# Kernel tuning notes

Hardware: AMD Instinct MI355X
Metric: run time of the kernel (lower is better)

Reference implementation:

```python
import jax, jax.numpy as jnp
import numpy as np

B, T, DM, H, DH = 4, 2048, 1024, 16, 64
DI = H * DH
CLIP = 1.0
LN_EPS = 1e-5


def setup_inputs() -> dict:
    key = jax.random.key(0)
    ks = jax.random.split(key, 9)

    def xav(k, shape):  # xavier_uniform, fan_in=shape[1], fan_out=shape[0]
        lim = float(np.sqrt(6.0 / (shape[0] + shape[1])))
        return jax.random.uniform(k, shape, jnp.float32, -lim, lim)

    def kai(k, shape):  # default nn.Linear weight init
        lim = float(1.0 / np.sqrt(shape[1]))
        return jax.random.uniform(k, shape, jnp.float32, -lim, lim)

    return {
        "x": jax.random.normal(ks[0], (B, T, DM), jnp.float32),
        "Wq": xav(ks[1], (DI, DM)),
        "Wk": xav(ks[2], (DI, DM)),
        "Wv": xav(ks[3], (DI, DM)),
        "Wa": kai(ks[4], (DI, DM)), "ba": jnp.full((DI,), 3.0, jnp.float32),
        "Wb": kai(ks[5], (H, DM)), "bb": jnp.zeros((H,), jnp.float32),
        "Wg": kai(ks[6], (H, DM)), "bg": jnp.zeros((H,), jnp.float32),
        "WaR": kai(ks[7], (DI, DM)), "baR": jnp.full((DI,), 3.0, jnp.float32),
        "Wo": xav(ks[8], (DM, DI)),
        "ln_w": jnp.ones((DM,), jnp.float32),
        "ln_b": jnp.zeros((DM,), jnp.float32),
    }


def reference(x, Wq, Wk, Wv, Wa, ba, Wb, bb, Wg, bg, WaR, baR, Wo, ln_w, ln_b):
    Bs, Ts, _ = x.shape
    residual = x
    # LayerNorm
    mu = jnp.mean(x, -1, keepdims=True)
    var = jnp.mean((x - mu) ** 2, -1, keepdims=True)
    xn = (x - mu) / jnp.sqrt(var + LN_EPS) * ln_w + ln_b

    q = (xn @ Wq.T).reshape(Bs, Ts, H, DH)
    k = (xn @ Wk.T).reshape(Bs, Ts, H, DH)
    v = (xn @ Wv.T).reshape(Bs, Ts, H, DH)
    alpha = jax.nn.sigmoid(xn @ Wa.T + ba).reshape(Bs, Ts, H, DH)
    aR = jax.nn.sigmoid(xn @ WaR.T + baR).reshape(Bs, Ts, H, DH)
    beta = jax.nn.sigmoid(xn @ Wb.T + bb)   # (B,T,H)
    gamma = jax.nn.sigmoid(xn @ Wg.T + bg)  # (B,T,H)

    tm = lambda a: jnp.moveaxis(a, 1, 0)  # time-major for scan
    xs = (tm(q), tm(k), tm(v), tm(alpha), tm(aR), tm(beta), tm(gamma))
    S0 = jnp.zeros((Bs, H, DH, DH), x.dtype)

    def step(carry, inp):
        S, R = carry
        q_t, k_t, v_t, a_t, aR_t, b_t, g_t = inp  # (B,H,d) / (B,H)
        kn = k_t / jnp.maximum(jnp.linalg.norm(k_t, axis=-1, keepdims=True), 1e-12)
        # residual target from previous state: r = clip(v - S^T k)
        pred = jnp.einsum('bhji,bhj->bhi', S, kn)
        r = jnp.clip(v_t - pred, -CLIP, CLIP)
        # primary state: S = diag(alpha) S; S += beta k (v - k^T S)
        S = a_t[..., None] * S
        kp = jnp.einsum('bhd,bhde->bhe', kn, S)
        S = S + b_t[..., None, None] * kn[..., None] * (v_t - kp)[..., None, :]
        o = jnp.einsum('bhji,bhj->bhi', S, q_t)
        # residual state
        R = aR_t[..., None] * R
        kpR = jnp.einsum('bhd,bhde->bhe', kn, R)
        R = R + g_t[..., None, None] * kn[..., None] * (r - kpR)[..., None, :]
        o = o + jnp.einsum('bhji,bhj->bhi', R, q_t)
        return (S, R), o

    _, os = jax.lax.scan(step, (S0, S0), xs)  # os: (T,B,H,d)
    out = jnp.moveaxis(os, 0, 1).reshape(Bs, Ts, DI) @ Wo.T
    return out + residual  # dropout is identity at inference
```

## Files before the change

### kernel.cpp

```cpp
#include <hip/hip_runtime.h>
#include <hip/hip_fp16.h>

#define B_SZ 4
#define T_SEQ 2048
#define NH 16
#define HD 64
#define DMODEL 1024
#define MTOT (B_SZ * T_SEQ)

typedef __bf16 bf16x8 __attribute__((ext_vector_type(8)));
typedef float f32x4 __attribute__((ext_vector_type(4)));
typedef float f32x2 __attribute__((ext_vector_type(2)));
typedef _Float16 f16x4 __attribute__((ext_vector_type(4)));

__device__ __forceinline__ unsigned short f2bf(float f) {
    union { float f; unsigned int i; } c; c.f = f;
    unsigned int u = c.i;
    u += 0x7fffu + ((u >> 16) & 1u);
    return (unsigned short)(u >> 16);
}
__device__ __forceinline__ float sigm(float x) { return 1.f / (1.f + __expf(-x)); }

__device__ __forceinline__ void dma16(const void* g, void* l) {
    __builtin_amdgcn_global_load_lds(
        (const __attribute__((address_space(1))) void*)g,
        (__attribute__((address_space(3))) void*)l, 16, 0, 0);
}

template <int CTRL>
__device__ __forceinline__ float dppadd(float x) {
    int v = __builtin_amdgcn_update_dpp(0, __builtin_bit_cast(int, x), CTRL, 0xf, 0xf, false);
    return x + __builtin_bit_cast(float, v);
}
__device__ __forceinline__ float rowsum16(float x) {
    x = dppadd<0x128>(x);
    x = dppadd<0x124>(x);
    x = dppadd<0x122>(x);
    x = dppadd<0x121>(x);
    return x;
}

__global__ __launch_bounds__(256, 1) void k_ln(const float* __restrict__ x,
                                               const float* __restrict__ lnw,
                                               const float* __restrict__ lnb,
                                               unsigned short* __restrict__ xn) {
    const int m = blockIdx.x;
    const int t = threadIdx.x;
    float4 xv = ((const float4*)(x + (size_t)m * DMODEL))[t];
    float s = xv.x + xv.y + xv.z + xv.w;
    float s2 = xv.x * xv.x + xv.y * xv.y + xv.z * xv.z + xv.w * xv.w;
#pragma unroll
    for (int off = 32; off >= 1; off >>= 1) {
        s += __shfl_xor(s, off);
        s2 += __shfl_xor(s2, off);
    }
    __shared__ float red[8];
    const int wid = t >> 6;
    if ((t & 63) == 0) { red[wid] = s; red[4 + wid] = s2; }
    __syncthreads();
    if (t == 0) {
        float su = red[0] + red[1] + red[2] + red[3];
        float sq = red[4] + red[5] + red[6] + red[7];
        float mu = su * (1.f / DMODEL);
        float var = sq * (1.f / DMODEL) - mu * mu;
        red[0] = mu;
        red[1] = rsqrtf(var + 1e-5f);
    }
    __syncthreads();
    float mu = red[0], rstd = red[1];
    float4 w4 = ((const float4*)lnw)[t];
    float4 b4 = ((const float4*)lnb)[t];
    ushort4 o;
    o.x = f2bf((xv.x - mu) * rstd * w4.x + b4.x);
    o.y = f2bf((xv.y - mu) * rstd * w4.y + b4.y);
    o.z = f2bf((xv.z - mu) * rstd * w4.z + b4.z);
    o.w = f2bf((xv.w - mu) * rstd * w4.w + b4.w);
    ((ushort4*)(xn + (size_t)m * DMODEL))[t] = o;
}

struct WPtrs { const float* p0; const float* p1; const float* p2; const float* p3; const float* p4; };

__global__ __launch_bounds__(256, 1) void k_wconv(WPtrs w, unsigned short* __restrict__ dst) {
    const int plane = blockIdx.y;
    const float* src = plane == 0 ? w.p0 : plane == 1 ? w.p1 : plane == 2 ? w.p2
                                                             : plane == 3 ? w.p3 : w.p4;
    const size_t i = ((size_t)blockIdx.x * 256 + threadIdx.x) * 8;
    float4 f0 = *(const float4*)(src + i);
    float4 f1 = *(const float4*)(src + i + 4);
    uint4 o;
    o.x = (unsigned)f2bf(f0.x) | ((unsigned)f2bf(f0.y) << 16);
    o.y = (unsigned)f2bf(f0.z) | ((unsigned)f2bf(f0.w) << 16);
    o.z = (unsigned)f2bf(f1.x) | ((unsigned)f2bf(f1.y) << 16);
    o.w = (unsigned)f2bf(f1.z) | ((unsigned)f2bf(f1.w) << 16);
    *(uint4*)(dst + (size_t)plane * 1048576 + i) = o;
}

__global__ __launch_bounds__(256, 1) void k_cvt1(const float* __restrict__ src,
                                                 unsigned short* __restrict__ dst) {
    const size_t i = ((size_t)blockIdx.x * 256 + threadIdx.x) * 8;
    float4 f0 = *(const float4*)(src + i);
    float4 f1 = *(const float4*)(src + i + 4);
    uint4 o;
    o.x = (unsigned)f2bf(f0.x) | ((unsigned)f2bf(f0.y) << 16);
    o.y = (unsigned)f2bf(f0.z) | ((unsigned)f2bf(f0.w) << 16);
    o.z = (unsigned)f2bf(f1.x) | ((unsigned)f2bf(f1.y) << 16);
    o.w = (unsigned)f2bf(f1.z) | ((unsigned)f2bf(f1.w) << 16);
    *(uint4*)(dst + i) = o;
}

template <int KDIM>
__device__ __forceinline__ void gemm128(const unsigned short* __restrict__ A,
                                        const unsigned short* __restrict__ Bw,
                                        int m0, int n0, f32x4 acc[4][4]) {
    __shared__ __align__(16) unsigned short sA[128 * 32];
    __shared__ __align__(16) unsigned short sB[128 * 32];

    const int t = threadIdx.x;
    const int lane = t & 63;
    const int wv = t >> 6;
    const int wm = wv >> 1, wn = wv & 1;
    const int ml = lane & 15, kq = lane >> 4;

#pragma unroll
    for (int i = 0; i < 4; i++)
#pragma unroll
        for (int j = 0; j < 4; j++) {
            f32x4 z; z[0] = 0.f; z[1] = 0.f; z[2] = 0.f; z[3] = 0.f;
            acc[i][j] = z;
        }

    const unsigned short* pA = A + (size_t)m0 * KDIM;
    const unsigned short* pB = Bw + (size_t)n0 * KDIM;
    const unsigned short* gA0 = pA + (size_t)(t >> 2) * KDIM + (t & 3) * 8;
    const unsigned short* gA1 = gA0 + (size_t)64 * KDIM;
    const unsigned short* gB0 = pB + (size_t)(t >> 2) * KDIM + (t & 3) * 8;
    const unsigned short* gB1 = gB0 + (size_t)64 * KDIM;
    unsigned short* lA0 = sA + wv * 512;
    unsigned short* lA1 = lA0 + 2048;
    unsigned short* lB0 = sB + wv * 512;
    unsigned short* lB1 = lB0 + 2048;

    for (int kb = 0; kb < KDIM / 32; kb++) {
        const int ko = kb * 32;
        dma16(gA0 + ko, lA0);
        dma16(gA1 + ko, lA1);
        dma16(gB0 + ko, lB0);
        dma16(gB1 + ko, lB1);
        __syncthreads();
        bf16x8 af[4], bfr[4];
#pragma unroll
        for (int mt = 0; mt < 4; mt++)
            af[mt] = *(const bf16x8*)&sA[(wm * 64 + mt * 16 + ml) * 32 + kq * 8];
#pragma unroll
        for (int nt = 0; nt < 4; nt++)
            bfr[nt] = *(const bf16x8*)&sB[(wn * 64 + nt * 16 + ml) * 32 + kq * 8];
#pragma unroll
        for (int mt = 0; mt < 4; mt++)
#pragma unroll
            for (int nt = 0; nt < 4; nt++)
                acc[mt][nt] = __builtin_amdgcn_mfma_f32_16x16x32_bf16(af[mt], bfr[nt], acc[mt][nt], 0, 0, 0);
        __syncthreads();
    }
}

__global__ __launch_bounds__(256, 1) void k_proj(const unsigned short* __restrict__ xn,
                                                 const unsigned short* __restrict__ wbf,
                                                 const float* __restrict__ ba,
                                                 const float* __restrict__ baR,
                                                 __half* __restrict__ qo, __half* __restrict__ ko,
                                                 __half* __restrict__ vo, __half* __restrict__ ao,
                                                 __half* __restrict__ aRo) {
    const int m0 = blockIdx.x * 128;
    const int yt = blockIdx.y;
    const int widx = yt >> 3;
    const int n0 = (yt & 7) * 128;
    const unsigned short* W = wbf + (size_t)widx * 1048576;
    f32x4 acc[4][4];
    gemm128<1024>(xn, W, m0, n0, acc);

    __half* outp = widx == 0 ? qo : widx == 1 ? ko : widx == 2 ? vo : widx == 3 ? ao : aRo;
    const float* bias = (widx == 3) ? ba : (widx == 4) ? baR : (const float*)0;
    const int lane = threadIdx.x & 63;
    const int wv = threadIdx.x >> 6;
    const int wm = wv >> 1, wn = wv & 1;
    const int ml = lane & 15, kq = lane >> 4;
#pragma unroll
    for (int mt = 0; mt < 4; mt++)
#pragma unroll
        for (int nt = 0; nt < 4; nt++) {
            const int rowg = m0 + wm * 64 + mt * 16 + kq * 4;
            const int colg = n0 + wn * 64 + nt * 16 + ml;
            float bval = bias ? bias[colg] : 0.f;
#pragma unroll
            for (int r = 0; r < 4; r++) {
                float v = acc[mt][nt][r];
                if (widx >= 3) v = sigm(v + bval);
                outp[(size_t)(rowg + r) * DMODEL + colg] = __float2half(v);
            }
        }
}

__global__ __launch_bounds__(256, 1) void k_bg(const unsigned short* __restrict__ xn,
                                               const float* __restrict__ Wb,
                                               const float* __restrict__ bb,
                                               const float* __restrict__ Wg,
                                               const float* __restrict__ bgp,
                                               f32x2* __restrict__ bgpk) {
    const int m = blockIdx.x;
    const int t = threadIdx.x;
    const int h = t >> 4, seg = t & 15;
    const ushort4* xr = (const ushort4*)(xn + (size_t)m * DMODEL + seg * 64);
    const float4* wbr = (const float4*)(Wb + (size_t)h * DMODEL + seg * 64);
    const float4* wgr = (const float4*)(Wg + (size_t)h * DMODEL + seg * 64);
    float db = 0.f, dg = 0.f;
#pragma unroll
    for (int u = 0; u < 16; u++) {
        ushort4 a = xr[u];
        float4 w1 = wbr[u], w2 = wgr[u];
        union { unsigned int i; float f; } c0, c1, c2, c3;
        c0.i = ((unsigned int)a.x) << 16; c1.i = ((unsigned int)a.y) << 16;
        c2.i = ((unsigned int)a.z) << 16; c3.i = ((unsigned int)a.w) << 16;
        db += c0.f * w1.x + c1.f * w1.y + c2.f * w1.z + c3.f * w1.w;
        dg += c0.f * w2.x + c1.f * w2.y + c2.f * w2.z + c3.f * w2.w;
    }
#pragma unroll
    for (int off = 1; off < 16; off <<= 1) {
        db += __shfl_xor(db, off);
        dg += __shfl_xor(dg, off);
    }
    if (seg == 0) {
        f32x2 o;
        o[0] = sigm(db + bb[h]);
        o[1] = sigm(dg + bgp[h]);
        bgpk[(size_t)m * NH + h] = o;
    }
}

__global__ __launch_bounds__(256, 1) void k_prep(__half* __restrict__ kb) {
    const int row = blockIdx.x * 16 + (threadIdx.x >> 4);
    const int tr = threadIdx.x & 15;
    const int bh = row >> 11, t = row & 2047;
    const size_t idx = ((size_t)((bh >> 4) * T_SEQ + t)) * DMODEL + (bh & 15) * 64 + tr * 4;
    f16x4 k4 = *(const f16x4*)((const __half*)kb + idx);
    float k0 = (float)k4[0], k1 = (float)k4[1], k2 = (float)k4[2], k3 = (float)k4[3];
    float ss = k0 * k0 + k1 * k1 + k2 * k2 + k3 * k3;
    ss = rowsum16(ss);
    float inv = 1.f / fmaxf(sqrtf(ss), 1e-12f);
    f16x4 o;
    o[0] = (_Float16)(k0 * inv); o[1] = (_Float16)(k1 * inv);
    o[2] = (_Float16)(k2 * inv); o[3] = (_Float16)(k3 * inv);
    *(f16x4*)(kb + idx) = o;
}

__global__ __launch_bounds__(256, 1) void k_scan(const __half* __restrict__ qb,
                                                 const __half* __restrict__ knb,
                                                 const __half* __restrict__ vb,
                                                 const __half* __restrict__ ab,
                                                 const __half* __restrict__ aRb,
                                                 const f32x2* __restrict__ bgpk,
                                                 unsigned short* __restrict__ ob) {
    const int blk = blockIdx.x;
    const int bh = blk & 63, cg = blk >> 6;
    const int b = bh >> 4, h = bh & 15;
    const int t = threadIdx.x;
    const int col = t >> 4, tr = t & 15;
    const int ii = cg * 16 + col;
    const int j0 = tr * 4;

    const size_t vecbase = ((size_t)b * T_SEQ) * DMODEL + h * 64 + j0;
    const size_t vbase = ((size_t)b * T_SEQ) * DMODEL + h * 64 + ii;
    const size_t bgbase = ((size_t)b * T_SEQ) * NH + h;

    const __half* pk = knb + vecbase;
    const __half* pq = qb + vecbase;
    const __half* pa = ab + vecbase;
    const __half* pr = aRb + vecbase;

    float S0 = 0, S1 = 0, S2 = 0, S3 = 0, R0 = 0, R1 = 0, R2 = 0, R3 = 0;

    f16x4 rk[6], rq[6], ra[6], rr[6];
    __half rv[6];
    f32x2 rbg[6];
    f32x4 fkn[6], fq[6], fa[6], fr[6];
    float fv[6];

#pragma unroll
    for (int p = 0; p < 6; p++) {
        const size_t voff = (size_t)p * DMODEL;
        rk[p] = *(const f16x4*)(pk + voff);
        rq[p] = *(const f16x4*)(pq + voff);
        ra[p] = *(const f16x4*)(pa + voff);
        rr[p] = *(const f16x4*)(pr + voff);
        rv[p] = vb[vbase + voff];
        rbg[p] = bgpk[bgbase + (size_t)p * NH];
    }
    fkn[0][0] = (float)rk[0][0]; fkn[0][1] = (float)rk[0][1]; fkn[0][2] = (float)rk[0][2]; fkn[0][3] = (float)rk[0][3];
    fq[0][0] = (float)rq[0][0]; fq[0][1] = (float)rq[0][1]; fq[0][2] = (float)rq[0][2]; fq[0][3] = (float)rq[0][3];
    fa[0][0] = (float)ra[0][0]; fa[0][1] = (float)ra[0][1]; fa[0][2] = (float)ra[0][2]; fa[0][3] = (float)ra[0][3];
    fr[0][0] = (float)rr[0][0]; fr[0][1] = (float)rr[0][1]; fr[0][2] = (float)rr[0][2]; fr[0][3] = (float)rr[0][3];
    fv[0] = (float)rv[0];

#define SCAN_BODY(P, PN)                                                              \
    {                                                                                 \
        const int s = st + (P);                                                       \
        const float beta = rbg[P][0], gamma = rbg[P][1];                              \
                     \
        {                                                                             \
            const size_t voff = (size_t)((s + 6) & (T_SEQ - 1)) * DMODEL;             \
            rk[P] = *(const f16x4*)(pk + voff);                                       \
            rq[P] = *(const f16x4*)(pq + voff);                                       \
            ra[P] = *(const f16x4*)(pa + voff);                                       \
            rr[P] = *(const f16x4*)(pr + voff);                                       \
            rv[P] = vb[vbase + voff];                                                 \
        }                                                                             \
                                    \
        fkn[PN][0] = (float)rk[PN][0]; fkn[PN][1] = (float)rk[PN][1];                 \
        fkn[PN][2] = (float)rk[PN][2]; fkn[PN][3] = (float)rk[PN][3];                 \
        fq[PN][0] = (float)rq[PN][0]; fq[PN][1] = (float)rq[PN][1];                   \
        fq[PN][2] = (float)rq[PN][2]; fq[PN][3] = (float)rq[PN][3];                   \
        fa[PN][0] = (float)ra[PN][0]; fa[PN][1] = (float)ra[PN][1];                   \
        fa[PN][2] = (float)ra[PN][2]; fa[PN][3] = (float)ra[PN][3];                   \
        fr[PN][0] = (float)rr[PN][0]; fr[PN][1] = (float)rr[PN][1];                   \
        fr[PN][2] = (float)rr[PN][2]; fr[PN][3] = (float)rr[PN][3];                   \
        fv[PN] = (float)rv[PN];                                                       \
                                          \
        {                                                                             \
            const float kn0 = fkn[P][0], kn1 = fkn[P][1], kn2 = fkn[P][2], kn3 = fkn[P][3]; \
            const float a0 = fa[P][0], a1 = fa[P][1], a2 = fa[P][2], a3 = fa[P][3];   \
            const float x0 = fr[P][0], x1 = fr[P][1], x2 = fr[P][2], x3 = fr[P][3];   \
            const float vc = fv[P];                                                   \
            float pred = S0 * kn0 + S1 * kn1 + S2 * kn2 + S3 * kn3;                   \
            float Sd0 = a0 * S0, Sd1 = a1 * S1, Sd2 = a2 * S2, Sd3 = a3 * S3;         \
            float Rd0 = x0 * R0, Rd1 = x1 * R1, Rd2 = x2 * R2, Rd3 = x3 * R3;         \
            float kp = Sd0 * kn0 + Sd1 * kn1 + Sd2 * kn2 + Sd3 * kn3;                 \
            float kpR = Rd0 * kn0 + Rd1 * kn1 + Rd2 * kn2 + Rd3 * kn3;                \
            pred = rowsum16(pred);                                                    \
            kp = rowsum16(kp);                                                        \
            kpR = rowsum16(kpR);                                                      \
            const float rres = fminf(fmaxf(vc - pred, -1.f), 1.f);                    \
            const float cS = beta * (vc - kp);                                        \
            const float cR = gamma * (rres - kpR);                                    \
            S0 = fmaf(cS, kn0, Sd0); S1 = fmaf(cS, kn1, Sd1);                         \
            S2 = fmaf(cS, kn2, Sd2); S3 = fmaf(cS, kn3, Sd3);                         \
            R0 = fmaf(cR, kn0, Rd0); R1 = fmaf(cR, kn1, Rd1);                         \
            R2 = fmaf(cR, kn2, Rd2); R3 = fmaf(cR, kn3, Rd3);                         \
            float o = (S0 + R0) * fq[P][0] + (S1 + R1) * fq[P][1] +                   \
                      (S2 + R2) * fq[P][2] + (S3 + R3) * fq[P][3];                    \
            o = rowsum16(o);                                                          \
            if (tr == 0 && s < T_SEQ)                                                 \
                ob[vbase + (size_t)s * DMODEL] = f2bf(o);                             \
        }                                                                             \
             \
        rbg[P] = bgpk[bgbase + (size_t)((s + 6) & (T_SEQ - 1)) * NH];                 \
    }

    for (int st = 0; st < T_SEQ; st += 6) {
        SCAN_BODY(0, 1)
        SCAN_BODY(1, 2)
        SCAN_BODY(2, 3)
        SCAN_BODY(3, 4)
        SCAN_BODY(4, 5)
        SCAN_BODY(5, 0)
    }
#undef SCAN_BODY
}

__global__ __launch_bounds__(256, 1) void k_out(const unsigned short* __restrict__ ob,
                                                const unsigned short* __restrict__ wobf,
                                                const float* __restrict__ x,
                                                float* __restrict__ out) {
    const int m0 = blockIdx.x * 128;
    const int n0 = blockIdx.y * 128;
    f32x4 acc[4][4];
    gemm128<1024>(ob, wobf, m0, n0, acc);
    const int lane = threadIdx.x & 63;
    const int wv = threadIdx.x >> 6;
    const int wm = wv >> 1, wn = wv & 1;
    const int ml = lane & 15, kq = lane >> 4;
#pragma unroll
    for (int mt = 0; mt < 4; mt++)
#pragma unroll
        for (int nt = 0; nt < 4; nt++) {
            const int rowg = m0 + wm * 64 + mt * 16 + kq * 4;
            const int colg = n0 + wn * 64 + nt * 16 + ml;
#pragma unroll
            for (int r = 0; r < 4; r++) {
                size_t idx = (size_t)(rowg + r) * DMODEL + colg;
                out[idx] = acc[mt][nt][r] + x[idx];
            }
        }
}

extern "C" void kernel_launch(void* const* d_in, const int* in_sizes, int n_in,
                              void* d_out, int out_size, void* d_ws, size_t ws_size,
                              hipStream_t stream) {
    const float* x = (const float*)d_in[0];
    const float* Wq = (const float*)d_in[1];
    const float* Wk = (const float*)d_in[2];
    const float* Wv = (const float*)d_in[3];
    const float* Wa = (const float*)d_in[4];
    const float* ba = (const float*)d_in[5];
    const float* Wb = (const float*)d_in[6];
    const float* bb = (const float*)d_in[7];
    const float* Wg = (const float*)d_in[8];
    const float* bg = (const float*)d_in[9];
    const float* WaR = (const float*)d_in[10];
    const float* baR = (const float*)d_in[11];
    const float* Wo = (const float*)d_in[12];
    const float* lnw = (const float*)d_in[13];
    const float* lnb = (const float*)d_in[14];

    const size_t SZ = 16777216ULL;
    size_t need = 6 * SZ + 2 * 1048576ULL;
    if (ws_size < need) return;

    char* ws = (char*)d_ws;
    __half* qb = (__half*)(ws + 0 * SZ);
    __half* kb = (__half*)(ws + 1 * SZ);
    __half* vb = (__half*)(ws + 2 * SZ);
    __half* ab = (__half*)(ws + 3 * SZ);
    __half* aRb = (__half*)(ws + 4 * SZ);
    unsigned short* xn = (unsigned short*)(ws + 5 * SZ);
    f32x2* bgpk = (f32x2*)(ws + 6 * SZ);

    unsigned short* wbf = (unsigned short*)d_out;
    unsigned short* wobf = (unsigned short*)qb;

    WPtrs wp{Wq, Wk, Wv, Wa, WaR};
    k_wconv<<<dim3(512, 5), dim3(256), 0, stream>>>(wp, wbf);
    k_ln<<<dim3(MTOT), dim3(256), 0, stream>>>(x, lnw, lnb, xn);
    k_proj<<<dim3(64, 40), dim3(256), 0, stream>>>(xn, wbf, ba, baR, qb, kb, vb, ab, aRb);
    k_bg<<<dim3(MTOT), dim3(256), 0, stream>>>(xn, Wb, bb, Wg, bg, bgpk);
    k_prep<<<dim3(MTOT * NH / 16), dim3(256), 0, stream>>>(kb);
    k_scan<<<dim3(256), dim3(256), 0, stream>>>(qb, kb, vb, ab, aRb, bgpk, xn);
    k_cvt1<<<dim3(512), dim3(256), 0, stream>>>(Wo, wobf);
    k_out<<<dim3(64, 8), dim3(256), 0, stream>>>(xn, wobf, x, (float*)d_out);
}
```

Before: 944.4 us.

## Run recurrent scan on MFMA with fp16 state in single wavefront blocks

The scan kernel now runs each 16-column state slice in one 64-lane wavefront instead of a 256-thread block. State S and R are held as fp16 vectors (16 rows per lane across 4 quads). The k^T S, k^T R and q^T S dot products use 16x16x32 fp16 MFMA instructions in place of DPP row reductions. This cuts the per-step cross-lane reduction latency on the serial critical path. The trade-off is fp16 storage of the recurrent state, which risks accumulated precision loss over 2048 steps, and MFMA issue latency on each step.

```diff
diff --git a/kernel.cpp b/kernel.cpp
--- a/kernel.cpp
+++ b/kernel.cpp
@@ -12,6 +12,7 @@
 typedef float f32x4 __attribute__((ext_vector_type(4)));
 typedef float f32x2 __attribute__((ext_vector_type(2)));
 typedef _Float16 f16x4 __attribute__((ext_vector_type(4)));
+typedef _Float16 f16x8 __attribute__((ext_vector_type(8)));
 
 __device__ __forceinline__ unsigned short f2bf(float f) {
     union { float f; unsigned int i; } c; c.f = f;
@@ -252,117 +253,86 @@
     *(f16x4*)(kb + idx) = o;
 }
 
-__global__ __launch_bounds__(256, 1) void k_scan(const __half* __restrict__ qb,
-                                                 const __half* __restrict__ knb,
-                                                 const __half* __restrict__ vb,
-                                                 const __half* __restrict__ ab,
-                                                 const __half* __restrict__ aRb,
-                                                 const f32x2* __restrict__ bgpk,
-                                                 unsigned short* __restrict__ ob) {
+__global__ __launch_bounds__(64, 1) void k_scan(const __half* __restrict__ qb,
+                                                const __half* __restrict__ knb,
+                                                const __half* __restrict__ vb,
+                                                const __half* __restrict__ ab,
+                                                const __half* __restrict__ aRb,
+                                                const f32x2* __restrict__ bgpk,
+                                                unsigned short* __restrict__ ob) {
     const int blk = blockIdx.x;
     const int bh = blk & 63, cg = blk >> 6;
     const int b = bh >> 4, h = bh & 15;
-    const int t = threadIdx.x;
-    const int col = t >> 4, tr = t & 15;
+    const int l = threadIdx.x;
+    const int col = l & 15, quad = l >> 4;
     const int ii = cg * 16 + col;
-    const int j0 = tr * 4;
-
-    const size_t vecbase = ((size_t)b * T_SEQ) * DMODEL + h * 64 + j0;
-    const size_t vbase = ((size_t)b * T_SEQ) * DMODEL + h * 64 + ii;
-    const size_t bgbase = ((size_t)b * T_SEQ) * NH + h;
-
-    const __half* pk = knb + vecbase;
-    const __half* pq = qb + vecbase;
-    const __half* pa = ab + vecbase;
-    const __half* pr = aRb + vecbase;
-
-    float S0 = 0, S1 = 0, S2 = 0, S3 = 0, R0 = 0, R1 = 0, R2 = 0, R3 = 0;
-
-    f16x4 rk[6], rq[6], ra[6], rr[6];
-    __half rv[6];
-    f32x2 rbg[6];
-    f32x4 fkn[6], fq[6], fa[6], fr[6];
-    float fv[6];
-
-#pragma unroll
-    for (int p = 0; p < 6; p++) {
-        const size_t voff = (size_t)p * DMODEL;
-        rk[p] = *(const f16x4*)(pk + voff);
-        rq[p] = *(const f16x4*)(pq + voff);
-        ra[p] = *(const f16x4*)(pa + voff);
-        rr[p] = *(const f16x4*)(pr + voff);
-        rv[p] = vb[vbase + voff];
-        rbg[p] = bgpk[bgbase + (size_t)p * NH];
-    }
-    fkn[0][0] = (float)rk[0][0]; fkn[0][1] = (float)rk[0][1]; fkn[0][2] = (float)rk[0][2]; fkn[0][3] = (float)rk[0][3];
-    fq[0][0] = (float)rq[0][0]; fq[0][1] = (float)rq[0][1]; fq[0][2] = (float)rq[0][2]; fq[0][3] = (float)rq[0][3];
-    fa[0][0] = (float)ra[0][0]; fa[0][1] = (float)ra[0][1]; fa[0][2] = (float)ra[0][2]; fa[0][3] = (float)ra[0][3];
-    fr[0][0] = (float)rr[0][0]; fr[0][1] = (float)rr[0][1]; fr[0][2] = (float)rr[0][2]; fr[0][3] = (float)rr[0][3];
-    fv[0] = (float)rv[0];
-
-#define SCAN_BODY(P, PN)                                                              \
-    {                                                                                 \
-        const int s = st + (P);                                                       \
-        const float beta = rbg[P][0], gamma = rbg[P][1];                              \
-                     \
-        {                                                                             \
-            const size_t voff = (size_t)((s + 6) & (T_SEQ - 1)) * DMODEL;             \
-            rk[P] = *(const f16x4*)(pk + voff);                                       \
-            rq[P] = *(const f16x4*)(pq + voff);                                       \
-            ra[P] = *(const f16x4*)(pa + voff);                                       \
-            rr[P] = *(const f16x4*)(pr + voff);                                       \
-            rv[P] = vb[vbase + voff];                                                 \
-        }                                                                             \
-                                    \
-        fkn[PN][0] = (float)rk[PN][0]; fkn[PN][1] = (float)rk[PN][1];                 \
-        fkn[PN][2] = (float)rk[PN][2]; fkn[PN][3] = (float)rk[PN][3];                 \
-        fq[PN][0] = (float)rq[PN][0]; fq[PN][1] = (float)rq[PN][1];                   \
-        fq[PN][2] = (float)rq[PN][2]; fq[PN][3] = (float)rq[PN][3];                   \
-        fa[PN][0] = (float)ra[PN][0]; fa[PN][1] = (float)ra[PN][1];                   \
-        fa[PN][2] = (float)ra[PN][2]; fa[PN][3] = (float)ra[PN][3];                   \
-        fr[PN][0] = (float)rr[PN][0]; fr[PN][1] = (float)rr[PN][1];                   \
-        fr[PN][2] = (float)rr[PN][2]; fr[PN][3] = (float)rr[PN][3];                   \
-        fv[PN] = (float)rv[PN];                                                       \
-                                          \
-        {                                                                             \
-            const float kn0 = fkn[P][0], kn1 = fkn[P][1], kn2 = fkn[P][2], kn3 = fkn[P][3]; \
-            const float a0 = fa[P][0], a1 = fa[P][1], a2 = fa[P][2], a3 = fa[P][3];   \
-            const float x0 = fr[P][0], x1 = fr[P][1], x2 = fr[P][2], x3 = fr[P][3];   \
-            const float vc = fv[P];                                                   \
-            float pred = S0 * kn0 + S1 * kn1 + S2 * kn2 + S3 * kn3;                   \
-            float Sd0 = a0 * S0, Sd1 = a1 * S1, Sd2 = a2 * S2, Sd3 = a3 * S3;         \
-            float Rd0 = x0 * R0, Rd1 = x1 * R1, Rd2 = x2 * R2, Rd3 = x3 * R3;         \
-            float kp = Sd0 * kn0 + Sd1 * kn1 + Sd2 * kn2 + Sd3 * kn3;                 \
-            float kpR = Rd0 * kn0 + Rd1 * kn1 + Rd2 * kn2 + Rd3 * kn3;                \
-            pred = rowsum16(pred);                                                    \
-            kp = rowsum16(kp);                                                        \
-            kpR = rowsum16(kpR);                                                      \
-            const float rres = fminf(fmaxf(vc - pred, -1.f), 1.f);                    \
-            const float cS = beta * (vc - kp);                                        \
-            const float cR = gamma * (rres - kpR);                                    \
-            S0 = fmaf(cS, kn0, Sd0); S1 = fmaf(cS, kn1, Sd1);                         \
-            S2 = fmaf(cS, kn2, Sd2); S3 = fmaf(cS, kn3, Sd3);                         \
-            R0 = fmaf(cR, kn0, Rd0); R1 = fmaf(cR, kn1, Rd1);                         \
-            R2 = fmaf(cR, kn2, Rd2); R3 = fmaf(cR, kn3, Rd3);                         \
-            float o = (S0 + R0) * fq[P][0] + (S1 + R1) * fq[P][1] +                   \
-                      (S2 + R2) * fq[P][2] + (S3 + R3) * fq[P][3];                    \
-            o = rowsum16(o);                                                          \
-            if (tr == 0 && s < T_SEQ)                                                 \
-                ob[vbase + (size_t)s * DMODEL] = f2bf(o);                             \
-        }                                                                             \
-             \
-        rbg[P] = bgpk[bgbase + (size_t)((s + 6) & (T_SEQ - 1)) * NH];                 \
-    }
-
-    for (int st = 0; st < T_SEQ; st += 6) {
-        SCAN_BODY(0, 1)
-        SCAN_BODY(1, 2)
-        SCAN_BODY(2, 3)
-        SCAN_BODY(3, 4)
-        SCAN_BODY(4, 5)
-        SCAN_BODY(5, 0)
-    }
-#undef SCAN_BODY
+
+    const size_t base = (size_t)b * T_SEQ * DMODEL + h * 64;
+    const __half* pk = knb + base + quad * 8;
+    const __half* pq = qb + base + quad * 8;
+    const __half* pa = ab + base + quad * 8;
+    const __half* pr = aRb + base + quad * 8;
+    const __half* pv = vb + base + ii;
+    unsigned short* po = ob + base + ii;
+    const size_t bgbase = (size_t)b * T_SEQ * NH + h;
+
+    f16x8 SL = (f16x8)(_Float16)0, SH = (f16x8)(_Float16)0;
+    f16x8 RL = (f16x8)(_Float16)0, RH = (f16x8)(_Float16)0;
+
+    struct In {
+        f16x8 knL, knH, aL, aH, xL, xH, qL, qH;
+        float vc;
+        f32x2 bg;
+    };
+
+    auto load = [&](int s) {
+        In r;
+        const size_t vo = (size_t)s * DMODEL;
+        r.knL = *(const f16x8*)(pk + vo); r.knH = *(const f16x8*)(pk + vo + 32);
+        r.aL = *(const f16x8*)(pa + vo);  r.aH = *(const f16x8*)(pa + vo + 32);
+        r.xL = *(const f16x8*)(pr + vo);  r.xH = *(const f16x8*)(pr + vo + 32);
+        r.qL = *(const f16x8*)(pq + vo);  r.qH = *(const f16x8*)(pq + vo + 32);
+        r.vc = (float)pv[vo];
+        r.bg = bgpk[bgbase + (size_t)s * NH];
+        return r;
+    };
+
+    auto step = [&](const In& c, int s) {
+        f32x4 z; z[0] = 0.f; z[1] = 0.f; z[2] = 0.f; z[3] = 0.f;
+        f32x4 pA1 = __builtin_amdgcn_mfma_f32_16x16x32_f16(c.knL, SL, z, 0, 0, 0);
+        f32x4 pA2 = __builtin_amdgcn_mfma_f32_16x16x32_f16(c.knH, SH, z, 0, 0, 0);
+        f16x8 SdL = c.aL * SL, SdH = c.aH * SH;
+        f16x8 RdL = c.xL * RL, RdH = c.xH * RH;
+        f32x4 kA1 = __builtin_amdgcn_mfma_f32_16x16x32_f16(c.knL, SdL, z, 0, 0, 0);
+        f32x4 kA2 = __builtin_amdgcn_mfma_f32_16x16x32_f16(c.knH, SdH, z, 0, 0, 0);
+        f32x4 rA1 = __builtin_amdgcn_mfma_f32_16x16x32_f16(c.knL, RdL, z, 0, 0, 0);
+        f32x4 rA2 = __builtin_amdgcn_mfma_f32_16x16x32_f16(c.knH, RdH, z, 0, 0, 0);
+        const float pred = pA1[0] + pA2[0];
+        const float kp = kA1[0] + kA2[0];
+        const float kpR = rA1[0] + rA2[0];
+        const float rres = fminf(fmaxf(c.vc - pred, -1.f), 1.f);
+        const float cS = c.bg[0] * (c.vc - kp);
+        const float cR = c.bg[1] * (rres - kpR);
+        const _Float16 csh = (_Float16)cS;
+        const _Float16 crh = (_Float16)cR;
+        const f16x8 csv = {csh, csh, csh, csh, csh, csh, csh, csh};
+        const f16x8 crv = {crh, crh, crh, crh, crh, crh, crh, crh};
+        SL = SdL + csv * c.knL; SH = SdH + csv * c.knH;
+        RL = RdL + crv * c.knL; RH = RdH + crv * c.knH;
+        f16x8 TL = SL + RL, TH = SH + RH;
+        f32x4 oA1 = __builtin_amdgcn_mfma_f32_16x16x32_f16(c.qL, TL, z, 0, 0, 0);
+        f32x4 oA2 = __builtin_amdgcn_mfma_f32_16x16x32_f16(c.qH, TH, z, 0, 0, 0);
+        if (quad == 0)
+            po[(size_t)s * DMODEL] = f2bf(oA1[0] + oA2[0]);
+    };
+
+    In bufA = load(0), bufB;
+    for (int s = 0; s < T_SEQ; s += 2) {
+        bufB = load((s + 1) & (T_SEQ - 1));
+        step(bufA, s);
+        bufA = load((s + 2) & (T_SEQ - 1));
+        step(bufB, s + 1);
+    }
 }
 
 __global__ __launch_bounds__(256, 1) void k_out(const unsigned short* __restrict__ ob,
@@ -432,7 +402,7 @@
     k_proj<<<dim3(64, 40), dim3(256), 0, stream>>>(xn, wbf, ba, baR, qb, kb, vb, ab, aRb);
     k_bg<<<dim3(MTOT), dim3(256), 0, stream>>>(xn, Wb, bb, Wg, bg, bgpk);
     k_prep<<<dim3(MTOT * NH / 16), dim3(256), 0, stream>>>(kb);
-    k_scan<<<dim3(256), dim3(256), 0, stream>>>(qb, kb, vb, ab, aRb, bgpk, xn);
+    k_scan<<<dim3(256), dim3(64), 0, stream>>>(qb, kb, vb, ab, aRb, bgpk, xn);
     k_cvt1<<<dim3(512), dim3(256), 0, stream>>>(Wo, wobf);
     k_out<<<dim3(64, 8), dim3(256), 0, stream>>>(xn, wobf, x, (float*)d_out);
 }
```

Result: slower. 1.213 ms (+28.4%).
